# Performance work log

Hardware: AMD Instinct MI355X
Metric: run time of the kernel (lower is better)

The kernel has to match this reference:

```python
import jax, jax.numpy as jnp
import numpy as np

L = 4          # num layers
NH = 128       # hidden channels per layer
FC = 16        # frame_channel = patch^2 * C
HP = 32        # H / patch
WP = 32        # W / patch
K = 5          # filter_size
B = 8
T_PREV = 10
T_AFTER = 10
T_TOTAL = T_PREV + T_AFTER - 1  # 19 generated frames
FORGET_BIAS = 1.0


def _conv(x, w):
    # x: [B, Cin, H, W], w: [Cout, Cin, kh, kw], stride 1, SAME padding
    return jax.lax.conv_general_dilated(
        x, w, (1, 1), 'SAME', dimension_numbers=('NCHW', 'OIHW', 'NCHW'))


def _st_lstm_cell(x, h, c, m, Wx, Wh, Wm, Wo, Wl):
    # Standard PredRNN SpatioTemporalLSTMCell (bias-free convs, no layer norm)
    xc = _conv(x, Wx)   # [B, 7*NH, H, W]
    hc = _conv(h, Wh)   # [B, 4*NH, H, W]
    mc = _conv(m, Wm)   # [B, 3*NH, H, W]
    i_x, f_x, g_x, i_xp, f_xp, g_xp, o_x = jnp.split(xc, 7, axis=1)
    i_h, f_h, g_h, o_h = jnp.split(hc, 4, axis=1)
    i_m, f_m, g_m = jnp.split(mc, 3, axis=1)

    i_t = jax.nn.sigmoid(i_x + i_h)
    f_t = jax.nn.sigmoid(f_x + f_h + FORGET_BIAS)
    g_t = jnp.tanh(g_x + g_h)
    c_new = f_t * c + i_t * g_t

    i_tp = jax.nn.sigmoid(i_xp + i_m)
    f_tp = jax.nn.sigmoid(f_xp + f_m + FORGET_BIAS)
    g_tp = jnp.tanh(g_xp + g_m)
    m_new = f_tp * m + i_tp * g_tp

    mem = jnp.concatenate([c_new, m_new], axis=1)  # [B, 2*NH, H, W]
    o_t = jax.nn.sigmoid(o_x + o_h + _conv(mem, Wo))
    h_new = o_t * jnp.tanh(_conv(mem, Wl))
    return h_new, c_new, m_new


def setup_inputs() -> dict:
    key = jax.random.key(0)
    ks = jax.random.split(key, 9)
    s = jnp.float32(0.02)  # small init scale to keep gates in a sane range
    return {
        'frames_tensor': jax.random.normal(ks[0], (B, T_PREV + T_AFTER, HP, WP, FC), jnp.float32),
        'mask_true': jax.random.uniform(ks[1], (B, T_AFTER - 1, HP, WP, FC), jnp.float32),
        'Wx0': jax.random.normal(ks[2], (7 * NH, FC, K, K), jnp.float32) * s,
        'Wx': jax.random.normal(ks[3], (L - 1, 7 * NH, NH, K, K), jnp.float32) * s,
        'Wh': jax.random.normal(ks[4], (L, 4 * NH, NH, K, K), jnp.float32) * s,
        'Wm': jax.random.normal(ks[5], (L, 3 * NH, NH, K, K), jnp.float32) * s,
        'Wo': jax.random.normal(ks[6], (L, NH, 2 * NH, K, K), jnp.float32) * s,
        'Wl': jax.random.normal(ks[7], (L, NH, 2 * NH, 1, 1), jnp.float32) * s,
        'Wout': jax.random.normal(ks[8], (FC, NH, 1, 1), jnp.float32) * s,
    }


def reference(frames_tensor, mask_true, Wx0, Wx, Wh, Wm, Wo, Wl, Wout):
    # [B,T,H,W,C] -> [B,T,C,H,W]
    frames = jnp.transpose(frames_tensor, (0, 1, 4, 2, 3))
    mask = jnp.transpose(mask_true, (0, 1, 4, 2, 3))

    # For t < data_previous the input is the ground-truth frame (mask == 1);
    # afterwards it is blended with the previous generation x_gen.
    ones = jnp.ones((B, T_PREV, FC, HP, WP), frames.dtype)
    mask_seq = jnp.concatenate([ones, mask], axis=1)  # [B, T_TOTAL, C, H, W]

    frames_t = jnp.transpose(frames[:, :T_TOTAL], (1, 0, 2, 3, 4))  # [T,B,C,H,W]
    mask_t = jnp.transpose(mask_seq, (1, 0, 2, 3, 4))               # [T,B,C,H,W]

    h0 = jnp.zeros((L, B, NH, HP, WP), frames.dtype)
    c0 = jnp.zeros((L, B, NH, HP, WP), frames.dtype)
    m0 = jnp.zeros((B, NH, HP, WP), frames.dtype)
    xg0 = jnp.zeros((B, FC, HP, WP), frames.dtype)

    def step(carry, xs):
        h, c, m, x_gen = carry
        frame, msk = xs
        net = msk * frame + (1.0 - msk) * x_gen
        h_new, c_new, m = _st_lstm_cell(net, h[0], c[0], m, Wx0, Wh[0], Wm[0], Wo[0], Wl[0])
        hs, cs = [h_new], [c_new]
        for i in range(1, L):
            hi, ci, m = _st_lstm_cell(hs[-1], h[i], c[i], m, Wx[i - 1], Wh[i], Wm[i], Wo[i], Wl[i])
            hs.append(hi)
            cs.append(ci)
        x_gen = _conv(hs[-1], Wout)  # 1x1 conv, no bias
        return (jnp.stack(hs), jnp.stack(cs), m, x_gen), x_gen

    _, next_frames = jax.lax.scan(step, (h0, c0, m0, xg0), (frames_t, mask_t))
    # [T,B,C,H,W] -> [B,T,H,W,C]
    return jnp.transpose(next_frames, (1, 0, 3, 4, 2))
```

## Files before the change

kernel.cpp:

```cpp
#include <hip/hip_runtime.h>
#include <math.h>

#define TT 19
#define TPREV 10

typedef __attribute__((ext_vector_type(8))) short bf8v;
typedef __attribute__((ext_vector_type(4))) float f4v;
typedef __attribute__((ext_vector_type(16))) float f16v;

__device__ __forceinline__ float sigmoidf_(float x){ return 1.f/(1.f+expf(-x)); }
__device__ __forceinline__ unsigned short f2bf(float x){
    unsigned int u = __float_as_uint(x);
    u += 0x7FFFu + ((u>>16)&1u);
    return (unsigned short)(u>>16);
}
__device__ __forceinline__ float bf2f(unsigned short b){ return __uint_as_float(((unsigned int)b)<<16); }

#define GLDS(g, l) __builtin_amdgcn_global_load_lds( \
    (const __attribute__((address_space(1))) void*)(g),   \
    (__attribute__((address_space(3))) void*)(l), 16, 0, 0)

struct HSeg {
    const unsigned short* in;
    int cl;
    int c0;
    int nch;
    int tap0, ntaps, five;
};
struct HJob {
    const unsigned short* wt;
    const unsigned short* w4;
    float* out;
    int cout_stride, pad;
    HSeg s;
};
struct HJobs14 { HJob j[14]; };
struct HJobs9  { HJob j[9]; };
struct HJobs7  { HJob j[7]; };

template<typename JOBS>
__global__ __launch_bounds__(256) void hconv_kernel(JOBS jobs, const unsigned short* zp)
{
    __shared__ unsigned short sA[8192];
    __shared__ unsigned short sH[12800];
    const HJob jb = jobs.j[blockIdx.y];
    const int tid = threadIdx.x;

    const int rA = tid & 127;
    const int q1 = tid >> 7;

    const int ng0 = blockIdx.x * 128;
    const int bb = ng0 >> 10, p0 = ng0 & 1023;
    const int y0 = p0 >> 5;

    const int lane = tid & 63, wv = tid >> 6;
    const int wm = (wv & 1) << 6;
    const int wn = (wv >> 1) << 6;
    const int col = lane & 31, ll5 = lane >> 5;

    int bofs0[2];
#pragma unroll
    for (int ni = 0; ni < 2; ++ni) {
        const int ln = wn + ni * 32 + col;
        bofs0[ni] = (((ln >> 5) + 2) * 40 + (ln & 31) + 4) * 40 + ll5 * 8;
    }

    f16v acc[2][2];
#pragma unroll
    for (int i = 0; i < 2; ++i)
#pragma unroll
        for (int j = 0; j < 2; ++j) acc[i][j] = (f16v)0.f;

    const HSeg sg = jb.s;

    if (sg.cl == 4) {
        const unsigned short* wrow4 = jb.w4 + (size_t)rA * 416 + q1 * 8;
        const unsigned short* inb4 = sg.in + ((size_t)bb << 14);
        const int pyy = y0 + (rA >> 5), pxx = rA & 31;
        for (int k = 0; k < 416; k += 32) {
            const unsigned short* gA = wrow4 + k;
            GLDS(gA,      &sA[tid * 8]);
            GLDS(gA + 16, &sA[(tid + 256) * 8]);
#pragma unroll
            for (int cc = 0; cc < 2; ++cc) {
                const int kk = k + q1 * 8 + cc * 16;
                const int tap = kk >> 4;
                const int ci = kk & 15;
                const int t5 = (tap * 52) >> 8;
                const int yy = pyy + t5 - 2;
                const int xx = pxx + (tap - t5 * 5) - 2;
                const bool ok = (tap < 25) & ((unsigned)yy < 32u) & ((unsigned)xx < 32u);
                const unsigned short* gp = ok ? (inb4 + ((((yy << 5) + xx)) << 4) + ci) : zp;
                GLDS(gp, cc ? &sH[(tid + 256) * 8] : &sH[tid * 8]);
            }
            __syncthreads();
#pragma unroll
            for (int s = 0; s < 2; ++s) {
                const int o = s * 2 + ll5;
                bf8v av[2], bv[2];
#pragma unroll
                for (int mi = 0; mi < 2; ++mi)
                    av[mi] = *(const bf8v*)&sA[(o * 128 + wm + mi * 32 + col) * 8];
#pragma unroll
                for (int ni = 0; ni < 2; ++ni)
                    bv[ni] = *(const bf8v*)&sH[(o * 128 + wn + ni * 32 + col) * 8];
#pragma unroll
                for (int mi = 0; mi < 2; ++mi)
#pragma unroll
                    for (int ni = 0; ni < 2; ++ni)
                        acc[mi][ni] = __builtin_amdgcn_mfma_f32_32x32x16_bf16(
                            av[mi], bv[ni], acc[mi][ni], 0, 0, 0);
            }
            __syncthreads();
        }
    } else {
        const unsigned short* inb = sg.in + ((size_t)bb << (10 + sg.cl));
        const unsigned short* wptr = jb.wt;
        int buf = 0;
        bool first = true;
        for (int ch = 0; ch < sg.nch; ++ch) {
            const int c0 = sg.c0 + ch * 32;
#pragma unroll
            for (int k = 0; k < 5; ++k) {
                const int s = tid + k * 256;
                const int r = s / 160;
                const int rem = s - r * 160;
                const int cc = rem >> 2, G = rem & 3;
                const int y = y0 + r - 2, x = cc - 4;
                const bool okv = ((unsigned)y < 32u) & ((unsigned)x < 32u);
                const int yc = okv ? y : 0, xc = okv ? x : 0;
                bf8v v = *(const bf8v*)(inb + ((((yc << 5) + xc)) << sg.cl) + c0 + G * 8);
                if (!okv) v = (bf8v)(short)0;
                *(bf8v*)&sH[(r * 40 + cc) * 40 + G * 8] = v;
            }
            if (first) {
                GLDS(wptr + tid * 8,         &sA[tid * 8]);
                GLDS(wptr + (tid + 256) * 8, &sA[(tid + 256) * 8]);
                wptr += 4096;
                first = false;
            }
            __syncthreads();
            for (int t = 0; t < sg.ntaps; ++t) {
                GLDS(wptr + tid * 8,         &sA[(buf ^ 1) * 4096 + tid * 8]);
                GLDS(wptr + (tid + 256) * 8, &sA[(buf ^ 1) * 4096 + (tid + 256) * 8]);
                wptr += 4096;
                int tapofs = 0;
                if (sg.five) {
                    const int tap = sg.tap0 + t;
                    const int t5 = (tap * 52) >> 8;
                    tapofs = ((t5 - 2) * 40 + (tap - t5 * 5 - 2)) * 40;
                }
                const unsigned short* sAb = &sA[buf * 4096];
#pragma unroll
                for (int s = 0; s < 2; ++s) {
                    const int o = s * 2 + ll5;
                    bf8v av[2], bv[2];
#pragma unroll
                    for (int mi = 0; mi < 2; ++mi)
                        av[mi] = *(const bf8v*)&sAb[(o * 128 + wm + mi * 32 + col) * 8];
#pragma unroll
                    for (int ni = 0; ni < 2; ++ni)
                        bv[ni] = *(const bf8v*)&sH[bofs0[ni] + tapofs + s * 16];
#pragma unroll
                    for (int mi = 0; mi < 2; ++mi)
#pragma unroll
                        for (int ni = 0; ni < 2; ++ni)
                            acc[mi][ni] = __builtin_amdgcn_mfma_f32_32x32x16_bf16(
                                av[mi], bv[ni], acc[mi][ni], 0, 0, 0);
                }
                __syncthreads();
                buf ^= 1;
            }
        }
    }

    const int nfix = ng0 + wn + col;
#pragma unroll
    for (int ni = 0; ni < 2; ++ni) {
        const int n = nfix + ni * 32;
        float* ob = jb.out + (size_t)n * jb.cout_stride;
#pragma unroll
        for (int mi = 0; mi < 2; ++mi) {
            const int mb = wm + mi * 32 + 4 * ll5;
            const f16v a = acc[mi][ni];
#pragma unroll
            for (int qd = 0; qd < 4; ++qd) {
                f4v v;
                v[0] = a[qd * 4 + 0]; v[1] = a[qd * 4 + 1];
                v[2] = a[qd * 4 + 2]; v[3] = a[qd * 4 + 3];
                *(f4v*)(ob + mb + qd * 8) = v;
            }
        }
    }
}

template<typename JOBS>
__global__ __launch_bounds__(256, 2) void hconvA_kernel(JOBS jobs, const unsigned short* zp)
{
    __shared__ unsigned short sA[16384];
    __shared__ unsigned short sH[19200];
    const int tid = threadIdx.x;

    const int nb   = gridDim.x * gridDim.y;
    const int per8 = nb >> 3;
    const int bidl = blockIdx.x + gridDim.x * blockIdx.y;
    const int g    = (bidl & 7) * per8 + (bidl >> 3);
    const int jy   = g >> 5;
    const int xt   = g & 31;
    const HJob jb = jobs.j[jy];

    const int ng0 = xt << 8;
    const int bb = ng0 >> 10, p0 = ng0 & 1023;
    const int y0 = p0 >> 5;

    const int lane = tid & 63, wv = tid >> 6;
    const int wm = (wv & 1) << 6;
    const int wn = (wv >> 1) << 7;
    const int col = lane & 31, ll5 = lane >> 5;

    int cell0[4];
#pragma unroll
    for (int ni = 0; ni < 4; ++ni) {
        const int ln = wn + ni * 32 + col;
        cell0[ni] = ((ln >> 5) + 2) * 40 + (ln & 31) + 4;
    }
    const int rowA0 = (wm + col) * 8;
    const int oA = ll5 * 1024;

    f16v acc[2][4];
#pragma unroll
    for (int i = 0; i < 2; ++i)
#pragma unroll
        for (int j = 0; j < 4; ++j) acc[i][j] = (f16v)0.f;

    const HSeg sg = jb.s;
    const unsigned short* inb = sg.in + ((size_t)bb << (10 + sg.cl));
    const unsigned short* wptr = jb.wt;
    const int ntaps = sg.ntaps;
    const int ntot = sg.nch * ntaps;

    {
        const int c0 = sg.c0;
#pragma unroll
        for (int k = 0; k < 8; ++k) {
            const int s = tid + k * 256;
            if (s < 1920) {
                const int r = s / 160;
                const int rem = s - r * 160;
                const int cc = rem >> 2, G = rem & 3;
                const int y = y0 + r - 2, x = cc - 4;
                const bool okv = ((unsigned)y < 32u) & ((unsigned)x < 32u);
                const int yc = okv ? y : 0, xc = okv ? x : 0;
                bf8v v = *(const bf8v*)(inb + ((((yc << 5) + xc)) << sg.cl) + c0 + G * 8);
                if (!okv) v = (bf8v)(short)0;
                const int cell = r * 40 + cc;
                *(bf8v*)&sH[cell * 40 + ((G ^ ((cell >> 3) & 3))) * 8] = v;
            }
        }
    }
    GLDS(wptr + tid * 8,                &sA[tid * 8]);
    GLDS(wptr + (tid + 256) * 8,        &sA[(tid + 256) * 8]);
    GLDS(wptr + 4096 + tid * 8,         &sA[4096 + tid * 8]);
    GLDS(wptr + 4096 + (tid + 256) * 8, &sA[4096 + (tid + 256) * 8]);
    wptr += 8192;

    int bcur = 0, tc = 0, ch = 0;
    for (int t = 0; t < ntot; ++t) {
        if (tc == ntaps) {
            tc = 0; ++ch;
            __syncthreads();
            const int c0 = sg.c0 + ch * 32;
#pragma unroll
            for (int k = 0; k < 8; ++k) {
                const int s = tid + k * 256;
                if (s < 1920) {
                    const int r = s / 160;
                    const int rem = s - r * 160;
                    const int cc = rem >> 2, G = rem & 3;
                    const int y = y0 + r - 2, x = cc - 4;
                    const bool okv = ((unsigned)y < 32u) & ((unsigned)x < 32u);
                    const int yc = okv ? y : 0, xc = okv ? x : 0;
                    bf8v v = *(const bf8v*)(inb + ((((yc << 5) + xc)) << sg.cl) + c0 + G * 8);
                    if (!okv) v = (bf8v)(short)0;
                    const int cell = r * 40 + cc;
                    *(bf8v*)&sH[cell * 40 + ((G ^ ((cell >> 3) & 3))) * 8] = v;
                }
            }
        }
        if (t + 2 < ntot) {
            const int b2 = (bcur + 2) & 3;
            GLDS(wptr + tid * 8,         &sA[b2 * 4096 + tid * 8]);
            GLDS(wptr + (tid + 256) * 8, &sA[b2 * 4096 + (tid + 256) * 8]);
            wptr += 4096;
        }
        int tapofs = 0;
        if (sg.five) {
            const int tap = sg.tap0 + tc;
            const int t5 = (tap * 52) >> 8;
            tapofs = (t5 - 2) * 40 + (tap - t5 * 5 - 2);
        }
        int baddr[4][2];
#pragma unroll
        for (int ni = 0; ni < 4; ++ni) {
            const int cT = cell0[ni] + tapofs;
            const int key = (cT >> 3) & 3;
            const int cb = cT * 40;
#pragma unroll
            for (int s = 0; s < 2; ++s)
                baddr[ni][s] = cb + (((s << 1) + ll5) ^ key) * 8;
        }
        if (t + 2 < ntot)      asm volatile("s_waitcnt vmcnt(4) lgkmcnt(0)" ::: "memory");
        else if (t + 1 < ntot) asm volatile("s_waitcnt vmcnt(2) lgkmcnt(0)" ::: "memory");
        else                   asm volatile("s_waitcnt vmcnt(0) lgkmcnt(0)" ::: "memory");
        __builtin_amdgcn_s_barrier();
        __builtin_amdgcn_sched_barrier(0);

        const unsigned short* sAb = &sA[bcur * 4096];
        bf8v av[2][2], bv[2][4];
#pragma unroll
        for (int s = 0; s < 2; ++s) {
#pragma unroll
            for (int mi = 0; mi < 2; ++mi)
                av[s][mi] = *(const bf8v*)&sAb[s * 2048 + oA + rowA0 + mi * 256];
#pragma unroll
            for (int ni = 0; ni < 4; ++ni)
                bv[s][ni] = *(const bf8v*)&sH[baddr[ni][s]];
        }
        __builtin_amdgcn_s_setprio(1);
#pragma unroll
        for (int s = 0; s < 2; ++s)
#pragma unroll
            for (int mi = 0; mi < 2; ++mi)
#pragma unroll
                for (int ni = 0; ni < 4; ++ni)
                    acc[mi][ni] = __builtin_amdgcn_mfma_f32_32x32x16_bf16(
                        av[s][mi], bv[s][ni], acc[mi][ni], 0, 0, 0);
        __builtin_amdgcn_s_setprio(0);
        __builtin_amdgcn_sched_barrier(0);

        bcur = (bcur + 1) & 3;
        ++tc;
    }

    const int nfix = ng0 + wn + col;
#pragma unroll
    for (int ni = 0; ni < 4; ++ni) {
        const int n = nfix + ni * 32;
        float* ob = jb.out + (size_t)n * jb.cout_stride;
#pragma unroll
        for (int mi = 0; mi < 2; ++mi) {
            const int mb = wm + mi * 32 + 4 * ll5;
            const f16v a = acc[mi][ni];
#pragma unroll
            for (int qd = 0; qd < 4; ++qd) {
                f4v v;
                v[0] = a[qd * 4 + 0]; v[1] = a[qd * 4 + 1];
                v[2] = a[qd * 4 + 2]; v[3] = a[qd * 4 + 3];
                *(f4v*)(ob + mb + qd * 8) = v;
            }
        }
    }
}

__global__ __launch_bounds__(256) void packT_kernel(
    const float* __restrict__ src, unsigned short* __restrict__ dst,
    int Cin, int srcTaps, int rowOff, int ci0, int ntaps, int tap0, int total)
{
    const int idx = blockIdx.x * 256 + threadIdx.x;
    if (idx >= total) return;
    const int j = idx & 7;
    const int row = (idx >> 3) & 127;
    const int q = (idx >> 10) & 3;
    const int at = idx >> 12;
    const int ch = at / ntaps;
    const int tap = tap0 + (at - ch * ntaps);
    const int ci = ci0 + ch * 32 + q * 8 + j;
    const float v = src[((size_t)(rowOff + row) * Cin + ci) * srcTaps + tap];
    dst[idx] = f2bf(v);
}

__global__ __launch_bounds__(256) void pack4_kernel(
    const float* __restrict__ src, unsigned short* __restrict__ dst, int total)
{
    const int idx = blockIdx.x * 256 + threadIdx.x;
    if (idx >= total) return;
    const int ci = idx & 15;
    const int t2 = idx >> 4;
    const int tap = t2 % 26;
    const int co = t2 / 26;
    float v = 0.f;
    if (tap < 25)
        v = src[((size_t)(co << 4) + ci) * 25 + tap];
    dst[idx] = f2bf(v);
}

__global__ __launch_bounds__(256) void net_kernel(
    const float* __restrict__ frames, const float* __restrict__ mask,
    const float* __restrict__ xgen, unsigned short* __restrict__ net, int t)
{
    const int idx = blockIdx.x * 256 + threadIdx.x;
    const int n = idx >> 4, ch = idx & 15;
    const int b = n >> 10, p = n & 1023;
    const float fr = frames[((((size_t)b * 20 + t) << 10) + p) * 16 + ch];
    float v;
    if (t < TPREV) v = fr;
    else {
        const float mk = mask[((((size_t)b * 9 + (t - TPREV)) << 10) + p) * 16 + ch];
        v = mk * fr + (1.f - mk) * xgen[idx];
    }
    net[idx] = f2bf(v);
}

__global__ __launch_bounds__(256) void gates_kernel(
    const float* __restrict__ preA, const float* __restrict__ preB,
    float* __restrict__ c, float* __restrict__ m,
    unsigned short* __restrict__ m_bf, unsigned short* __restrict__ mem)
{
    const int idx = blockIdx.x * 256 + threadIdx.x;
    const int n = idx >> 7, ch = idx & 127;
    const float* pa = preA + (size_t)n * 896 + ch;
    const float* pb = preB + (size_t)n * 896 + ch;
    const float i_ = pa[0]   + pb[0];
    const float f_ = pa[128] + pb[128];
    const float g_ = pa[256] + pb[256];
    const float ip = pa[384] + pb[384];
    const float fp = pa[512] + pb[512];
    const float gp = pa[640] + pb[640];
    const float cn = sigmoidf_(f_ + 1.f) * c[idx] + sigmoidf_(i_) * tanhf(g_);
    const float mn = sigmoidf_(fp + 1.f) * m[idx] + sigmoidf_(ip) * tanhf(gp);
    c[idx] = cn;
    m[idx] = mn;
    m_bf[idx] = f2bf(mn);
    mem[(size_t)n * 256 + ch] = f2bf(cn);
    mem[(size_t)n * 256 + 128 + ch] = f2bf(mn);
}

__global__ __launch_bounds__(256) void hout_kernel(
    const float* __restrict__ preA, const float* __restrict__ preB,
    const float* __restrict__ opart, const float* __restrict__ lconv,
    unsigned short* __restrict__ h)
{
    const int idx = blockIdx.x * 256 + threadIdx.x;
    const int n = idx >> 7, ch = idx & 127;
    float oc = preA[(size_t)n * 896 + 768 + ch] + preB[(size_t)n * 896 + 768 + ch];
#pragma unroll
    for (int j = 0; j < 8; ++j) oc += opart[idx + (size_t)j * 1048576];
    h[idx] = f2bf(sigmoidf_(oc) * tanhf(lconv[idx]));
}

__global__ __launch_bounds__(256) void wout_kernel(
    const unsigned short* __restrict__ h3, const float* __restrict__ wo,
    float* __restrict__ xgen, float* __restrict__ out, int t)
{
    const int idx = blockIdx.x * 256 + threadIdx.x;
    const int n = idx >> 4, ch = idx & 15;
    const int b = n >> 10, p = n & 1023;
    const unsigned short* hr = h3 + (size_t)n * 128;
    const float* wr = wo + ch * 128;
    float acc = 0.f;
#pragma unroll 8
    for (int ci = 0; ci < 128; ++ci)
        acc = fmaf(bf2f(hr[ci]), wr[ci], acc);
    xgen[idx] = acc;
    out[((((size_t)b * TT + t) << 10) + p) * 16 + ch] = acc;
}

extern "C" void kernel_launch(void* const* d_in, const int* in_sizes, int n_in,
                              void* d_out, int out_size, void* d_ws, size_t ws_size,
                              hipStream_t stream)
{
    const float* frames = (const float*)d_in[0];
    const float* mask   = (const float*)d_in[1];
    const float* Wx0    = (const float*)d_in[2];
    const float* Wx     = (const float*)d_in[3];
    const float* Wh     = (const float*)d_in[4];
    const float* Wm     = (const float*)d_in[5];
    const float* Wo     = (const float*)d_in[6];
    const float* Wl     = (const float*)d_in[7];
    const float* Wout   = (const float*)d_in[8];
    float* out = (float*)d_out;

    char* base = (char*)d_ws;
    size_t off = 0;
    auto take = [&](size_t bytes) -> char* {
        char* p = base + off;
        off = (off + bytes + 255) & ~(size_t)255;
        return p;
    };
    float* c0            = (float*)take(4ull * 1048576 * 4);
    float* m32           = (float*)take((size_t)1048576 * 4);
    unsigned short* hbf  = (unsigned short*)take(4ull * 1048576 * 2);
    unsigned short* mbf  = (unsigned short*)take((size_t)1048576 * 2);
    unsigned short* zp   = (unsigned short*)take(1024);
    const size_t zbytes = off;
    float* xgen          = (float*)take((size_t)131072 * 4);
    float* preA          = (float*)take((size_t)8192 * 896 * 4);
    float* preB          = (float*)take((size_t)8192 * 896 * 4);
    float* lconv         = (float*)take((size_t)1048576 * 4);
    float* opart         = (float*)take(8ull * 1048576 * 4);
    unsigned short* net  = (unsigned short*)take((size_t)131072 * 2);
    unsigned short* mem  = (unsigned short*)take((size_t)2097152 * 2);
    unsigned short* pa0x = (unsigned short*)take((size_t)896 * 416 * 2);
    unsigned short* paT0 = (unsigned short*)take(((size_t)7 * 100 * 4096 + 4096) * 2);
    unsigned short* paT1 = (unsigned short*)take(((size_t)7 * 200 * 4096 + 4096) * 2);
    unsigned short* paT2 = (unsigned short*)take(((size_t)7 * 200 * 4096 + 4096) * 2);
    unsigned short* paT3 = (unsigned short*)take(((size_t)7 * 200 * 4096 + 4096) * 2);
    unsigned short* paT[4] = { paT0, paT1, paT2, paT3 };
    unsigned short* oT   = (unsigned short*)take((4ull * 200 * 4096 + 4096) * 2);
    unsigned short* lT   = (unsigned short*)take((4ull * 8 * 4096 + 4096) * 2);

    hipMemsetAsync(d_ws, 0, zbytes, stream);

    auto packT = [&](const float* s, unsigned short* d, int Cin, int srcTaps,
                     int rowOff, int ci0, int nch, int ntaps, int tap0) {
        const int total = nch * ntaps * 4096;
        packT_kernel<<<(total + 255) / 256, 256, 0, stream>>>(
            s, d, Cin, srcTaps, rowOff, ci0, ntaps, tap0, total);
    };
    pack4_kernel<<<(896 * 416 + 255) / 256, 256, 0, stream>>>(Wx0, pa0x, 896 * 416);
    for (int g = 0; g < 7; ++g) {
        const float* hm0 = (g < 3) ? (Wh + (size_t)g * 128 * 128 * 25)
                         : (g == 6) ? (Wh + (size_t)384 * 128 * 25)
                                    : (Wm + (size_t)(g - 3) * 128 * 128 * 25);
        packT(hm0, paT0 + (size_t)g * 100 * 4096, 128, 25, 0, 0, 4, 25, 0);
        for (int l = 1; l < 4; ++l) {
            packT(Wx + (size_t)(l - 1) * 896 * 128 * 25,
                  paT[l] + (size_t)g * 200 * 4096, 128, 25, g * 128, 0, 4, 25, 0);
            const float* hmsrc = (g < 3) ? (Wh + ((size_t)l * 512 + g * 128) * 128 * 25)
                               : (g == 6) ? (Wh + ((size_t)l * 512 + 384) * 128 * 25)
                                          : (Wm + ((size_t)l * 384 + (g - 3) * 128) * 128 * 25);
            packT(hmsrc, paT[l] + ((size_t)g * 200 + 100) * 4096, 128, 25, 0, 0, 4, 25, 0);
        }
    }
    for (int l = 0; l < 4; ++l) {
        packT(Wo + (size_t)l * 128 * 256 * 25, oT + (size_t)l * 200 * 4096,
              256, 25, 0, 0, 8, 25, 0);
        packT(Wl + (size_t)l * 128 * 256, lT + (size_t)l * 8 * 4096,
              256, 1, 0, 0, 8, 1, 0);
    }

    for (int t = 0; t < TT; ++t) {
        net_kernel<<<512, 256, 0, stream>>>(frames, mask, xgen, net, t);
        for (int l = 0; l < 4; ++l) {
            unsigned short* hl = hbf + (size_t)l * 1048576;
            if (l == 0) {
                HJobs7 JG{}, JH{};
                for (int g = 0; g < 7; ++g) {
                    JG.j[g] = HJob{ pa0x, pa0x + (size_t)g * 128 * 416, preA + g * 128,
                                    896, 0, HSeg{ net, 4, 0, 0, 0, 0, 1 } };
                    const unsigned short* hmsrc = (g < 3 || g == 6) ? hl : mbf;
                    JH.j[g] = HJob{ paT0 + (size_t)g * 100 * 4096, nullptr, preB + g * 128,
                                    896, 0, HSeg{ hmsrc, 7, 0, 4, 0, 25, 1 } };
                }
                hconv_kernel<HJobs7><<<dim3(64, 7), 256, 0, stream>>>(JG, zp);
                hconvA_kernel<HJobs7><<<dim3(32, 7), 256, 0, stream>>>(JH, zp);
            } else {
                HJobs14 JA{};
                for (int g = 0; g < 7; ++g) {
                    const unsigned short* hmsrc = (g < 3 || g == 6) ? hl : mbf;
                    JA.j[g] = HJob{ paT[l] + (size_t)g * 200 * 4096, nullptr, preA + g * 128,
                                    896, 0, HSeg{ hbf + (size_t)(l - 1) * 1048576, 7, 0, 4, 0, 25, 1 } };
                    JA.j[7 + g] = HJob{ paT[l] + ((size_t)g * 200 + 100) * 4096, nullptr, preB + g * 128,
                                        896, 0, HSeg{ hmsrc, 7, 0, 4, 0, 25, 1 } };
                }
                hconvA_kernel<HJobs14><<<dim3(32, 14), 256, 0, stream>>>(JA, zp);
            }

            gates_kernel<<<4096, 256, 0, stream>>>(preA, preB,
                c0 + (size_t)l * 1048576, m32, mbf, mem);

            HJobs9 JB{};
            for (int jj = 0; jj < 8; ++jj)
                JB.j[jj] = HJob{ oT + ((size_t)l * 200 + jj * 25) * 4096, nullptr,
                                 opart + (size_t)jj * 1048576, 128, 0,
                                 HSeg{ mem, 8, jj * 32, 1, 0, 25, 1 } };
            JB.j[8] = HJob{ lT + (size_t)l * 8 * 4096, nullptr, lconv, 128, 0,
                            HSeg{ mem, 8, 0, 8, 0, 1, 0 } };
            hconv_kernel<HJobs9><<<dim3(64, 9), 256, 0, stream>>>(JB, zp);

            hout_kernel<<<4096, 256, 0, stream>>>(preA, preB, opart, lconv, hl);
        }
        wout_kernel<<<512, 256, 0, stream>>>(hbf + (size_t)3 * 1048576, Wout, xgen, out, t);
    }
}
```

Before: 11.32 ms.

## Unify convolutions on hconvA kernel, pad layer-0 input to 32 channels

Drops the separate hconv_kernel and its special 16-channel path. The layer-0 input is padded to 32 channels so the Wx0 conv runs through the generic packed-weight path, with the padded channels zeroed by a new ciMax argument to packT. Layer 0 now issues a single 14-job hconvA launch instead of two launches. The output and l convs also move to hconvA, using larger tiles and fewer blocks. This cuts launch count and reuses the tuned kernel, at the cost of wasted MACs on the zero-padded channels and less parallelism for the 9-job conv.

```diff
diff --git a/kernel.cpp b/kernel.cpp
--- a/kernel.cpp
+++ b/kernel.cpp
@@ -29,173 +29,15 @@
 };
 struct HJob {
     const unsigned short* wt;
-    const unsigned short* w4;
     float* out;
     int cout_stride, pad;
     HSeg s;
 };
 struct HJobs14 { HJob j[14]; };
 struct HJobs9  { HJob j[9]; };
-struct HJobs7  { HJob j[7]; };
 
 template<typename JOBS>
-__global__ __launch_bounds__(256) void hconv_kernel(JOBS jobs, const unsigned short* zp)
-{
-    __shared__ unsigned short sA[8192];
-    __shared__ unsigned short sH[12800];
-    const HJob jb = jobs.j[blockIdx.y];
-    const int tid = threadIdx.x;
-
-    const int rA = tid & 127;
-    const int q1 = tid >> 7;
-
-    const int ng0 = blockIdx.x * 128;
-    const int bb = ng0 >> 10, p0 = ng0 & 1023;
-    const int y0 = p0 >> 5;
-
-    const int lane = tid & 63, wv = tid >> 6;
-    const int wm = (wv & 1) << 6;
-    const int wn = (wv >> 1) << 6;
-    const int col = lane & 31, ll5 = lane >> 5;
-
-    int bofs0[2];
-#pragma unroll
-    for (int ni = 0; ni < 2; ++ni) {
-        const int ln = wn + ni * 32 + col;
-        bofs0[ni] = (((ln >> 5) + 2) * 40 + (ln & 31) + 4) * 40 + ll5 * 8;
-    }
-
-    f16v acc[2][2];
-#pragma unroll
-    for (int i = 0; i < 2; ++i)
-#pragma unroll
-        for (int j = 0; j < 2; ++j) acc[i][j] = (f16v)0.f;
-
-    const HSeg sg = jb.s;
-
-    if (sg.cl == 4) {
-        const unsigned short* wrow4 = jb.w4 + (size_t)rA * 416 + q1 * 8;
-        const unsigned short* inb4 = sg.in + ((size_t)bb << 14);
-        const int pyy = y0 + (rA >> 5), pxx = rA & 31;
-        for (int k = 0; k < 416; k += 32) {
-            const unsigned short* gA = wrow4 + k;
-            GLDS(gA,      &sA[tid * 8]);
-            GLDS(gA + 16, &sA[(tid + 256) * 8]);
-#pragma unroll
-            for (int cc = 0; cc < 2; ++cc) {
-                const int kk = k + q1 * 8 + cc * 16;
-                const int tap = kk >> 4;
-                const int ci = kk & 15;
-                const int t5 = (tap * 52) >> 8;
-                const int yy = pyy + t5 - 2;
-                const int xx = pxx + (tap - t5 * 5) - 2;
-                const bool ok = (tap < 25) & ((unsigned)yy < 32u) & ((unsigned)xx < 32u);
-                const unsigned short* gp = ok ? (inb4 + ((((yy << 5) + xx)) << 4) + ci) : zp;
-                GLDS(gp, cc ? &sH[(tid + 256) * 8] : &sH[tid * 8]);
-            }
-            __syncthreads();
-#pragma unroll
-            for (int s = 0; s < 2; ++s) {
-                const int o = s * 2 + ll5;
-                bf8v av[2], bv[2];
-#pragma unroll
-                for (int mi = 0; mi < 2; ++mi)
-                    av[mi] = *(const bf8v*)&sA[(o * 128 + wm + mi * 32 + col) * 8];
-#pragma unroll
-                for (int ni = 0; ni < 2; ++ni)
-                    bv[ni] = *(const bf8v*)&sH[(o * 128 + wn + ni * 32 + col) * 8];
-#pragma unroll
-                for (int mi = 0; mi < 2; ++mi)
-#pragma unroll
-                    for (int ni = 0; ni < 2; ++ni)
-                        acc[mi][ni] = __builtin_amdgcn_mfma_f32_32x32x16_bf16(
-                            av[mi], bv[ni], acc[mi][ni], 0, 0, 0);
-            }
-            __syncthreads();
-        }
-    } else {
-        const unsigned short* inb = sg.in + ((size_t)bb << (10 + sg.cl));
-        const unsigned short* wptr = jb.wt;
-        int buf = 0;
-        bool first = true;
-        for (int ch = 0; ch < sg.nch; ++ch) {
-            const int c0 = sg.c0 + ch * 32;
-#pragma unroll
-            for (int k = 0; k < 5; ++k) {
-                const int s = tid + k * 256;
-                const int r = s / 160;
-                const int rem = s - r * 160;
-                const int cc = rem >> 2, G = rem & 3;
-                const int y = y0 + r - 2, x = cc - 4;
-                const bool okv = ((unsigned)y < 32u) & ((unsigned)x < 32u);
-                const int yc = okv ? y : 0, xc = okv ? x : 0;
-                bf8v v = *(const bf8v*)(inb + ((((yc << 5) + xc)) << sg.cl) + c0 + G * 8);
-                if (!okv) v = (bf8v)(short)0;
-                *(bf8v*)&sH[(r * 40 + cc) * 40 + G * 8] = v;
-            }
-            if (first) {
-                GLDS(wptr + tid * 8,         &sA[tid * 8]);
-                GLDS(wptr + (tid + 256) * 8, &sA[(tid + 256) * 8]);
-                wptr += 4096;
-                first = false;
-            }
-            __syncthreads();
-            for (int t = 0; t < sg.ntaps; ++t) {
-                GLDS(wptr + tid * 8,         &sA[(buf ^ 1) * 4096 + tid * 8]);
-                GLDS(wptr + (tid + 256) * 8, &sA[(buf ^ 1) * 4096 + (tid + 256) * 8]);
-                wptr += 4096;
-                int tapofs = 0;
-                if (sg.five) {
-                    const int tap = sg.tap0 + t;
-                    const int t5 = (tap * 52) >> 8;
-                    tapofs = ((t5 - 2) * 40 + (tap - t5 * 5 - 2)) * 40;
-                }
-                const unsigned short* sAb = &sA[buf * 4096];
-#pragma unroll
-                for (int s = 0; s < 2; ++s) {
-                    const int o = s * 2 + ll5;
-                    bf8v av[2], bv[2];
-#pragma unroll
-                    for (int mi = 0; mi < 2; ++mi)
-                        av[mi] = *(const bf8v*)&sAb[(o * 128 + wm + mi * 32 + col) * 8];
-#pragma unroll
-                    for (int ni = 0; ni < 2; ++ni)
-                        bv[ni] = *(const bf8v*)&sH[bofs0[ni] + tapofs + s * 16];
-#pragma unroll
-                    for (int mi = 0; mi < 2; ++mi)
-#pragma unroll
-                        for (int ni = 0; ni < 2; ++ni)
-                            acc[mi][ni] = __builtin_amdgcn_mfma_f32_32x32x16_bf16(
-                                av[mi], bv[ni], acc[mi][ni], 0, 0, 0);
-                }
-                __syncthreads();
-                buf ^= 1;
-            }
-        }
-    }
-
-    const int nfix = ng0 + wn + col;
-#pragma unroll
-    for (int ni = 0; ni < 2; ++ni) {
-        const int n = nfix + ni * 32;
-        float* ob = jb.out + (size_t)n * jb.cout_stride;
-#pragma unroll
-        for (int mi = 0; mi < 2; ++mi) {
-            const int mb = wm + mi * 32 + 4 * ll5;
-            const f16v a = acc[mi][ni];
-#pragma unroll
-            for (int qd = 0; qd < 4; ++qd) {
-                f4v v;
-                v[0] = a[qd * 4 + 0]; v[1] = a[qd * 4 + 1];
-                v[2] = a[qd * 4 + 2]; v[3] = a[qd * 4 + 3];
-                *(f4v*)(ob + mb + qd * 8) = v;
-            }
-        }
-    }
-}
-
-template<typename JOBS>
-__global__ __launch_bounds__(256, 2) void hconvA_kernel(JOBS jobs, const unsigned short* zp)
+__global__ __launch_bounds__(256, 2) void hconvA_kernel(JOBS jobs)
 {
     __shared__ unsigned short sA[16384];
     __shared__ unsigned short sH[19200];
@@ -364,7 +206,8 @@
 
 __global__ __launch_bounds__(256) void packT_kernel(
     const float* __restrict__ src, unsigned short* __restrict__ dst,
-    int Cin, int srcTaps, int rowOff, int ci0, int ntaps, int tap0, int total)
+    int Cin, int srcTaps, int rowOff, int ci0, int ntaps, int tap0,
+    int ciMax, int total)
 {
     const int idx = blockIdx.x * 256 + threadIdx.x;
     if (idx >= total) return;
@@ -375,22 +218,9 @@
     const int ch = at / ntaps;
     const int tap = tap0 + (at - ch * ntaps);
     const int ci = ci0 + ch * 32 + q * 8 + j;
-    const float v = src[((size_t)(rowOff + row) * Cin + ci) * srcTaps + tap];
-    dst[idx] = f2bf(v);
-}
-
-__global__ __launch_bounds__(256) void pack4_kernel(
-    const float* __restrict__ src, unsigned short* __restrict__ dst, int total)
-{
-    const int idx = blockIdx.x * 256 + threadIdx.x;
-    if (idx >= total) return;
-    const int ci = idx & 15;
-    const int t2 = idx >> 4;
-    const int tap = t2 % 26;
-    const int co = t2 / 26;
     float v = 0.f;
-    if (tap < 25)
-        v = src[((size_t)(co << 4) + ci) * 25 + tap];
+    if (ci < ciMax)
+        v = src[((size_t)(rowOff + row) * Cin + ci) * srcTaps + tap];
     dst[idx] = f2bf(v);
 }
 
@@ -399,14 +229,16 @@
     const float* __restrict__ xgen, unsigned short* __restrict__ net, int t)
 {
     const int idx = blockIdx.x * 256 + threadIdx.x;
-    const int n = idx >> 4, ch = idx & 15;
-    const int b = n >> 10, p = n & 1023;
-    const float fr = frames[((((size_t)b * 20 + t) << 10) + p) * 16 + ch];
-    float v;
-    if (t < TPREV) v = fr;
-    else {
-        const float mk = mask[((((size_t)b * 9 + (t - TPREV)) << 10) + p) * 16 + ch];
-        v = mk * fr + (1.f - mk) * xgen[idx];
+    const int n = idx >> 5, ch = idx & 31;
+    float v = 0.f;
+    if (ch < 16) {
+        const int b = n >> 10, p = n & 1023;
+        const float fr = frames[((((size_t)b * 20 + t) << 10) + p) * 16 + ch];
+        if (t < TPREV) v = fr;
+        else {
+            const float mk = mask[((((size_t)b * 9 + (t - TPREV)) << 10) + p) * 16 + ch];
+            v = mk * fr + (1.f - mk) * xgen[(size_t)n * 16 + ch];
+        }
     }
     net[idx] = f2bf(v);
 }
@@ -491,16 +323,15 @@
     float* m32           = (float*)take((size_t)1048576 * 4);
     unsigned short* hbf  = (unsigned short*)take(4ull * 1048576 * 2);
     unsigned short* mbf  = (unsigned short*)take((size_t)1048576 * 2);
-    unsigned short* zp   = (unsigned short*)take(1024);
     const size_t zbytes = off;
     float* xgen          = (float*)take((size_t)131072 * 4);
     float* preA          = (float*)take((size_t)8192 * 896 * 4);
     float* preB          = (float*)take((size_t)8192 * 896 * 4);
     float* lconv         = (float*)take((size_t)1048576 * 4);
     float* opart         = (float*)take(8ull * 1048576 * 4);
-    unsigned short* net  = (unsigned short*)take((size_t)131072 * 2);
+    unsigned short* net  = (unsigned short*)take((size_t)262144 * 2);
     unsigned short* mem  = (unsigned short*)take((size_t)2097152 * 2);
-    unsigned short* pa0x = (unsigned short*)take((size_t)896 * 416 * 2);
+    unsigned short* pa0xT = (unsigned short*)take(((size_t)7 * 25 * 4096 + 4096) * 2);
     unsigned short* paT0 = (unsigned short*)take(((size_t)7 * 100 * 4096 + 4096) * 2);
     unsigned short* paT1 = (unsigned short*)take(((size_t)7 * 200 * 4096 + 4096) * 2);
     unsigned short* paT2 = (unsigned short*)take(((size_t)7 * 200 * 4096 + 4096) * 2);
@@ -512,71 +343,69 @@
     hipMemsetAsync(d_ws, 0, zbytes, stream);
 
     auto packT = [&](const float* s, unsigned short* d, int Cin, int srcTaps,
-                     int rowOff, int ci0, int nch, int ntaps, int tap0) {
+                     int rowOff, int ci0, int nch, int ntaps, int tap0, int ciMax) {
         const int total = nch * ntaps * 4096;
         packT_kernel<<<(total + 255) / 256, 256, 0, stream>>>(
-            s, d, Cin, srcTaps, rowOff, ci0, ntaps, tap0, total);
+            s, d, Cin, srcTaps, rowOff, ci0, ntaps, tap0, ciMax, total);
     };
-    pack4_kernel<<<(896 * 416 + 255) / 256, 256, 0, stream>>>(Wx0, pa0x, 896 * 416);
+    const int CIMAXBIG = 1 << 30;
     for (int g = 0; g < 7; ++g) {
+        packT(Wx0, pa0xT + (size_t)g * 25 * 4096, 16, 25, g * 128, 0, 1, 25, 0, 16);
         const float* hm0 = (g < 3) ? (Wh + (size_t)g * 128 * 128 * 25)
                          : (g == 6) ? (Wh + (size_t)384 * 128 * 25)
                                     : (Wm + (size_t)(g - 3) * 128 * 128 * 25);
-        packT(hm0, paT0 + (size_t)g * 100 * 4096, 128, 25, 0, 0, 4, 25, 0);
+        packT(hm0, paT0 + (size_t)g * 100 * 4096, 128, 25, 0, 0, 4, 25, 0, CIMAXBIG);
         for (int l = 1; l < 4; ++l) {
             packT(Wx + (size_t)(l - 1) * 896 * 128 * 25,
-                  paT[l] + (size_t)g * 200 * 4096, 128, 25, g * 128, 0, 4, 25, 0);
+                  paT[l] + (size_t)g * 200 * 4096, 128, 25, g * 128, 0, 4, 25, 0, CIMAXBIG);
             const float* hmsrc = (g < 3) ? (Wh + ((size_t)l * 512 + g * 128) * 128 * 25)
                                : (g == 6) ? (Wh + ((size_t)l * 512 + 384) * 128 * 25)
                                           : (Wm + ((size_t)l * 384 + (g - 3) * 128) * 128 * 25);
-            packT(hmsrc, paT[l] + ((size_t)g * 200 + 100) * 4096, 128, 25, 0, 0, 4, 25, 0);
+            packT(hmsrc, paT[l] + ((size_t)g * 200 + 100) * 4096, 128, 25, 0, 0, 4, 25, 0, CIMAXBIG);
         }
     }
     for (int l = 0; l < 4; ++l) {
         packT(Wo + (size_t)l * 128 * 256 * 25, oT + (size_t)l * 200 * 4096,
-              256, 25, 0, 0, 8, 25, 0);
+              256, 25, 0, 0, 8, 25, 0, CIMAXBIG);
         packT(Wl + (size_t)l * 128 * 256, lT + (size_t)l * 8 * 4096,
-              256, 1, 0, 0, 8, 1, 0);
+              256, 1, 0, 0, 8, 1, 0, CIMAXBIG);
     }
 
     for (int t = 0; t < TT; ++t) {
-        net_kernel<<<512, 256, 0, stream>>>(frames, mask, xgen, net, t);
+        net_kernel<<<1024, 256, 0, stream>>>(frames, mask, xgen, net, t);
         for (int l = 0; l < 4; ++l) {
             unsigned short* hl = hbf + (size_t)l * 1048576;
+            HJobs14 JA{};
             if (l == 0) {
-                HJobs7 JG{}, JH{};
-                for (int g = 0; g < 7; ++g) {
-                    JG.j[g] = HJob{ pa0x, pa0x + (size_t)g * 128 * 416, preA + g * 128,
-                                    896, 0, HSeg{ net, 4, 0, 0, 0, 0, 1 } };
-                    const unsigned short* hmsrc = (g < 3 || g == 6) ? hl : mbf;
-                    JH.j[g] = HJob{ paT0 + (size_t)g * 100 * 4096, nullptr, preB + g * 128,
-                                    896, 0, HSeg{ hmsrc, 7, 0, 4, 0, 25, 1 } };
-                }
-                hconv_kernel<HJobs7><<<dim3(64, 7), 256, 0, stream>>>(JG, zp);
-                hconvA_kernel<HJobs7><<<dim3(32, 7), 256, 0, stream>>>(JH, zp);
-            } else {
-                HJobs14 JA{};
                 for (int g = 0; g < 7; ++g) {
                     const unsigned short* hmsrc = (g < 3 || g == 6) ? hl : mbf;
-                    JA.j[g] = HJob{ paT[l] + (size_t)g * 200 * 4096, nullptr, preA + g * 128,
+                    JA.j[2 * g] = HJob{ pa0xT + (size_t)g * 25 * 4096, preA + g * 128,
+                                        896, 0, HSeg{ net, 5, 0, 1, 0, 25, 1 } };
+                    JA.j[2 * g + 1] = HJob{ paT0 + (size_t)g * 100 * 4096, preB + g * 128,
+                                            896, 0, HSeg{ hmsrc, 7, 0, 4, 0, 25, 1 } };
+                }
+            } else {
+                for (int g = 0; g < 7; ++g) {
+                    const unsigned short* hmsrc = (g < 3 || g == 6) ? hl : mbf;
+                    JA.j[g] = HJob{ paT[l] + (size_t)g * 200 * 4096, preA + g * 128,
                                     896, 0, HSeg{ hbf + (size_t)(l - 1) * 1048576, 7, 0, 4, 0, 25, 1 } };
-                    JA.j[7 + g] = HJob{ paT[l] + ((size_t)g * 200 + 100) * 4096, nullptr, preB + g * 128,
+                    JA.j[7 + g] = HJob{ paT[l] + ((size_t)g * 200 + 100) * 4096, preB + g * 128,
                                         896, 0, HSeg{ hmsrc, 7, 0, 4, 0, 25, 1 } };
                 }
-                hconvA_kernel<HJobs14><<<dim3(32, 14), 256, 0, stream>>>(JA, zp);
             }
+            hconvA_kernel<HJobs14><<<dim3(32, 14), 256, 0, stream>>>(JA);
 
             gates_kernel<<<4096, 256, 0, stream>>>(preA, preB,
                 c0 + (size_t)l * 1048576, m32, mbf, mem);
 
             HJobs9 JB{};
             for (int jj = 0; jj < 8; ++jj)
-                JB.j[jj] = HJob{ oT + ((size_t)l * 200 + jj * 25) * 4096, nullptr,
+                JB.j[jj] = HJob{ oT + ((size_t)l * 200 + jj * 25) * 4096,
                                  opart + (size_t)jj * 1048576, 128, 0,
                                  HSeg{ mem, 8, jj * 32, 1, 0, 25, 1 } };
-            JB.j[8] = HJob{ lT + (size_t)l * 8 * 4096, nullptr, lconv, 128, 0,
+            JB.j[8] = HJob{ lT + (size_t)l * 8 * 4096, lconv, 128, 0,
                             HSeg{ mem, 8, 0, 8, 0, 1, 0 } };
-            hconv_kernel<HJobs9><<<dim3(64, 9), 256, 0, stream>>>(JB, zp);
+            hconvA_kernel<HJobs9><<<dim3(32, 9), 256, 0, stream>>>(JB);
 
             hout_kernel<<<4096, 256, 0, stream>>>(preA, preB, opart, lconv, hl);
         }
```

Result: slower. 11.82 ms (+4.4%).
